# Performance work log

Hardware: AMD Instinct MI355X
Metric: run time of the kernel (lower is better)

## Reference

```python
import jax, jax.numpy as jnp
from jax import lax
import numpy as np

B, T, FEAT = 32, 256, 640
H, P = 2048, 640  # lstm_hidden_units, lstm_projection
FORGET_BIAS = 1.0  # TF v1 LSTMCell default


def setup_inputs() -> dict:
    key = jax.random.key(0)
    ks = jax.random.split(key, 6)
    s = 0.02  # small init so tanh/sigmoid stay well-conditioned
    return {
        "x": jax.random.normal(ks[0], (B, T, FEAT), dtype=jnp.float32),
        "W0": jax.random.normal(ks[1], (FEAT + P, 4 * H), dtype=jnp.float32) * s,
        "b0": jnp.zeros((4 * H,), dtype=jnp.float32),
        "P0": jax.random.normal(ks[2], (H, P), dtype=jnp.float32) * s,
        "W1": jax.random.normal(ks[3], (P + P, 4 * H), dtype=jnp.float32) * s,
        "b1": jnp.zeros((4 * H,), dtype=jnp.float32),
        "P1": jax.random.normal(ks[4], (H, P), dtype=jnp.float32) * s,
    }


def _lstmp_layer(x, W, b, proj):
    # x: [B, T, D]; TF v1 LSTMCell with num_proj, gate order (i, j, f, o)
    batch = x.shape[0]
    c0 = jnp.zeros((batch, H), dtype=x.dtype)
    m0 = jnp.zeros((batch, proj.shape[1]), dtype=x.dtype)

    def step(carry, xt):
        c, m = carry
        z = jnp.concatenate([xt, m], axis=-1) @ W + b  # [B, 4H]
        i, j, f, o = jnp.split(z, 4, axis=-1)
        c_new = jax.nn.sigmoid(f + FORGET_BIAS) * c + jax.nn.sigmoid(i) * jnp.tanh(j)
        m_new = (jax.nn.sigmoid(o) * jnp.tanh(c_new)) @ proj  # [B, P]
        return (c_new, m_new), m_new

    xT = jnp.swapaxes(x, 0, 1)  # [T, B, D]
    _, ys = lax.scan(step, (c0, m0), xT)
    return jnp.swapaxes(ys, 0, 1)  # [B, T, P]


def reference(x, W0, b0, P0, W1, b1, P1):
    h = _lstmp_layer(x, W0, b0, P0)
    h = _lstmp_layer(h, W1, b1, P1)
    return h
```

## Files before the change

kernel.cpp:

```cpp
#include <hip/hip_runtime.h>
#include <math.h>

typedef __attribute__((ext_vector_type(8))) short s16x8;
typedef __attribute__((ext_vector_type(8))) _Float16 f16x8;
typedef __attribute__((ext_vector_type(16))) float f32x16;
typedef unsigned long long u64;
typedef unsigned short u16;

#define NBLK 256
#define NTHR 512

constexpr int HSZ2 = 32 * 2048;
constexpr int MSZH = 32 * 640;

__device__ __forceinline__ float sigm(float v) { return 1.0f / (1.0f + expf(-v)); }

__device__ __forceinline__ unsigned short bf16_rne(float x) {
    unsigned u = __float_as_uint(x);
    return (unsigned short)((u + 0x7FFFu + ((u >> 16) & 1u)) >> 16);
}
__device__ __forceinline__ void split2(float x, unsigned short& hi, unsigned short& lo) {
    unsigned u = __float_as_uint(x);
    hi = (unsigned short)(u >> 16);
    float hf = __uint_as_float(u & 0xFFFF0000u);
    lo = bf16_rne(x - hf);
}
__device__ __forceinline__ void split8(const float* f, s16x8& h, s16x8& l) {
    #pragma unroll
    for (int i = 0; i < 8; ++i) {
        unsigned short hh, ll;
        split2(f[i], hh, ll);
        h[i] = (short)hh; l[i] = (short)ll;
    }
}

__device__ __forceinline__ void ast64(u16* p, u64 v) {
    __hip_atomic_store((u64*)p, v, __ATOMIC_RELAXED, __HIP_MEMORY_SCOPE_AGENT);
}
__device__ __forceinline__ void ast16(u16* p, u16 v) {
    __hip_atomic_store(p, v, __ATOMIC_RELAXED, __HIP_MEMORY_SCOPE_AGENT);
}

__device__ __forceinline__ void pollall(const unsigned* arr, unsigned e) {
    if (threadIdx.x < 64) {
        const int i0 = (int)threadIdx.x * 4;
        for (;;) {
            bool ok = (__hip_atomic_load(arr + i0 + 0, __ATOMIC_RELAXED, __HIP_MEMORY_SCOPE_AGENT) >= e) &&
                      (__hip_atomic_load(arr + i0 + 1, __ATOMIC_RELAXED, __HIP_MEMORY_SCOPE_AGENT) >= e) &&
                      (__hip_atomic_load(arr + i0 + 2, __ATOMIC_RELAXED, __HIP_MEMORY_SCOPE_AGENT) >= e) &&
                      (__hip_atomic_load(arr + i0 + 3, __ATOMIC_RELAXED, __HIP_MEMORY_SCOPE_AGENT) >= e);
            if (__all(ok)) break;
            __builtin_amdgcn_s_sleep(1);
        }
    }
    __syncthreads();
}

__global__ void transpose_split(const float* __restrict__ in,
                                u16* __restrict__ outHi, u16* __restrict__ outLo,
                                int R, int C) {
    __shared__ float tile[32][33];
    const int c0 = blockIdx.x * 32, r0 = blockIdx.y * 32;
    const int tid = threadIdx.x;
    {
        int r = tid >> 3, q = (tid & 7) * 4;
        float4 v = *(const float4*)(in + (size_t)(r0 + r) * C + c0 + q);
        tile[q + 0][r] = v.x; tile[q + 1][r] = v.y;
        tile[q + 2][r] = v.z; tile[q + 3][r] = v.w;
    }
    __syncthreads();
    {
        int c = tid >> 3, q = (tid & 7) * 4;
        ushort4 h, l;
        unsigned short hh, ll;
        split2(tile[c][q + 0], hh, ll); h.x = hh; l.x = ll;
        split2(tile[c][q + 1], hh, ll); h.y = hh; l.y = ll;
        split2(tile[c][q + 2], hh, ll); h.z = hh; l.z = ll;
        split2(tile[c][q + 3], hh, ll); h.w = hh; l.w = ll;
        size_t o = (size_t)(c0 + c) * R + r0 + q;
        *(ushort4*)(outHi + o) = h;
        *(ushort4*)(outLo + o) = l;
    }
}

__global__ void transpose_f16(const float* __restrict__ in, u16* __restrict__ outp,
                              int R, int C) {
    __shared__ float tile[32][33];
    const int c0 = blockIdx.x * 32, r0 = blockIdx.y * 32;
    const int tid = threadIdx.x;
    {
        int r = tid >> 3, q = (tid & 7) * 4;
        float4 v = *(const float4*)(in + (size_t)(r0 + r) * C + c0 + q);
        tile[q + 0][r] = v.x; tile[q + 1][r] = v.y;
        tile[q + 2][r] = v.z; tile[q + 3][r] = v.w;
    }
    __syncthreads();
    {
        int c = tid >> 3, q = (tid & 7) * 4;
        ushort4 o;
        o.x = __builtin_bit_cast(u16, (_Float16)tile[c][q + 0]);
        o.y = __builtin_bit_cast(u16, (_Float16)tile[c][q + 1]);
        o.z = __builtin_bit_cast(u16, (_Float16)tile[c][q + 2]);
        o.w = __builtin_bit_cast(u16, (_Float16)tile[c][q + 3]);
        *(ushort4*)(outp + (size_t)(c0 + c) * R + r0 + q) = o;
    }
}

__global__ void xcast(const float* __restrict__ in, u16* __restrict__ outp, int n4) {
    int i = blockIdx.x * blockDim.x + threadIdx.x;
    if (i < n4) {
        float4 v = ((const float4*)in)[i];
        ushort4 o;
        o.x = __builtin_bit_cast(u16, (_Float16)v.x);
        o.y = __builtin_bit_cast(u16, (_Float16)v.y);
        o.z = __builtin_bit_cast(u16, (_Float16)v.z);
        o.w = __builtin_bit_cast(u16, (_Float16)v.w);
        ((ushort4*)outp)[i] = o;
    }
}

__global__ void __launch_bounds__(256) qgemm(const float* __restrict__ P,
    const u16* __restrict__ WH, const u16* __restrict__ WL,
    u16* __restrict__ Qt) {
    const int tid = threadIdx.x;
    const int wid = tid >> 6, lane = tid & 63;
    const int n = lane & 31, kg = lane >> 5;
    const int tile = blockIdx.x * 4 + wid;
    const int ct = tile & 255, kt = tile >> 8;
    const int col = ct * 32 + n;
    const int krow = kt * 32 + n;

    f32x16 acc;
    #pragma unroll
    for (int r = 0; r < 16; ++r) acc[r] = 0.f;

    const float* ap = P + (size_t)krow * 640 + kg * 8;
    const u16* bhp = WH + (size_t)col * 1280 + 640 + kg * 8;
    const u16* blp = WL + (size_t)col * 1280 + 640 + kg * 8;
    #pragma unroll 4
    for (int ks = 0; ks < 40; ++ks) {
        float4 v0 = *(const float4*)(ap + ks * 16);
        float4 v1 = *(const float4*)(ap + ks * 16 + 4);
        float f[8] = {v0.x, v0.y, v0.z, v0.w, v1.x, v1.y, v1.z, v1.w};
        s16x8 ah, al;
        split8(f, ah, al);
        s16x8 bh = *(const s16x8*)(bhp + ks * 16);
        s16x8 bl = *(const s16x8*)(blp + ks * 16);
        acc = __builtin_amdgcn_mfma_f32_32x32x16_bf16(ah, bh, acc, 0, 0, 0);
        acc = __builtin_amdgcn_mfma_f32_32x32x16_bf16(ah, bl, acc, 0, 0, 0);
        acc = __builtin_amdgcn_mfma_f32_32x32x16_bf16(al, bh, acc, 0, 0, 0);
    }
    u16* qrow = Qt + (size_t)col * 2048 + kt * 32 + 4 * kg;
    #pragma unroll
    for (int q = 0; q < 4; ++q) {
        ushort4 o;
        o.x = __builtin_bit_cast(u16, (_Float16)acc[4 * q + 0]);
        o.y = __builtin_bit_cast(u16, (_Float16)acc[4 * q + 1]);
        o.z = __builtin_bit_cast(u16, (_Float16)acc[4 * q + 2]);
        o.w = __builtin_bit_cast(u16, (_Float16)acc[4 * q + 3]);
        *(ushort4*)(qrow + 8 * q) = o;
    }
}

__global__ void __launch_bounds__(NTHR, 2) lstm_pipe(
    const u16* __restrict__ xh,
    const float* __restrict__ bias0, const float* __restrict__ bias1,
    const u16* __restrict__ Wxt0, const u16* __restrict__ Wxt1,
    const u16* __restrict__ Qt0, const u16* __restrict__ Qt1,
    const u16* __restrict__ Pt0, const u16* __restrict__ Pt1,
    u16* __restrict__ hb0, u16* __restrict__ hb1,
    u16* __restrict__ m0r,
    float* out, unsigned* arr) {
    __shared__ float part[8][64][20];
    __shared__ float zb0[32][33];
    __shared__ float zb1[32][33];
    __shared__ u16 hst0[32][8];
    __shared__ u16 hst1[32][8];

    const int tid = threadIdx.x, bid = blockIdx.x;
    const int wid = tid >> 6, lane = tid & 63;
    const int n = lane & 31, kg = lane >> 5;

    const int colmap = (n >> 3) * 2048 + bid * 8 + (n & 7);
    const size_t wx640 = (size_t)colmap * 640 + wid * 80 + kg * 8;
    const size_t qOff  = (size_t)colmap * 2048 + wid * 256 + kg * 8;
    const size_t aXh   = (size_t)n * (256 * 640) + wid * 80 + kg * 8;
    const size_t aM    = (size_t)n * 640 + wid * 80 + kg * 8;
    const size_t hROff = (size_t)n * 2048 + wid * 256 + kg * 8;

    const int rn = tid >> 4, rm0 = (tid & 15) * 2;
    const int ch = tid >> 5, cb = tid & 31;

    const bool isL0t = bid < 40;
    const int  l0tb  = (bid < 20) ? bid : bid - 20;
    const int  l0par = (bid < 20) ? 0 : 1;
    const bool isL1t = (bid >= 40 && bid < 80);
    const int  l1tb  = (bid < 60) ? bid - 40 : bid - 60;
    const int  l1par = (bid < 60) ? 0 : 1;
    const size_t p0Off = (size_t)(l0tb * 32 + n) * 2048 + wid * 256 + kg * 8;
    const size_t p1Off = (size_t)(l1tb * 32 + n) * 2048 + wid * 256 + kg * 8;

    const float bv0 = bias0[(rn >> 3) * 2048 + bid * 8 + (rn & 7)];
    const float bv1 = bias1[(rn >> 3) * 2048 + bid * 8 + (rn & 7)];

    uint4 q0r[16], q1r[16];
    #pragma unroll
    for (int ks = 0; ks < 16; ++ks) {
        q0r[ks] = *(const uint4*)(Qt0 + qOff + ks * 16);
        q1r[ks] = *(const uint4*)(Qt1 + qOff + ks * 16);
    }
    #pragma unroll
    for (int ks = 0; ks < 16; ++ks) {
        asm volatile("" : "+v"(q0r[ks].x), "+v"(q0r[ks].y), "+v"(q0r[ks].z), "+v"(q0r[ks].w));
        asm volatile("" : "+v"(q1r[ks].x), "+v"(q1r[ks].y), "+v"(q1r[ks].z), "+v"(q1r[ks].w));
    }

    float creg0 = 0.f, creg1 = 0.f;

    auto xp0 = [&](int t) -> f32x16 {
        f32x16 a;
        #pragma unroll
        for (int r = 0; r < 16; ++r) a[r] = 0.f;
        const u16* xb = xh + aXh + (size_t)t * 640;
        const u16* wb = Wxt0 + wx640;
        #pragma unroll
        for (int ks = 0; ks < 5; ++ks)
            a = __builtin_amdgcn_mfma_f32_32x32x16_f16(*(const f16x8*)(xb + ks * 16),
                                                       *(const f16x8*)(wb + ks * 16), a, 0, 0, 0);
        return a;
    };
    auto xp1 = [&](int s) -> f32x16 {
        f32x16 a;
        #pragma unroll
        for (int r = 0; r < 16; ++r) a[r] = 0.f;
        const u16* mb = m0r + (size_t)s * MSZH + aM;
        const u16* wb = Wxt1 + wx640;
        #pragma unroll
        for (int ks = 0; ks < 5; ++ks)
            a = __builtin_amdgcn_mfma_f32_32x32x16_f16(*(const f16x8*)(mb + ks * 16),
                                                       *(const f16x8*)(wb + ks * 16), a, 0, 0, 0);
        return a;
    };
    auto stash = [&](const f32x16& v) {
        #pragma unroll
        for (int r = 0; r < 4; ++r) {
            float4 w;
            w.x = v[4 * r + 0]; w.y = v[4 * r + 1];
            w.z = v[4 * r + 2]; w.w = v[4 * r + 3];
            *(float4*)&part[wid][lane][4 * r] = w;
        }
    };
    auto sum8 = [&](int m) -> float {
        int lp = rn + 32 * ((m >> 2) & 1);
        int rg = (m & 3) + 4 * (m >> 3);
        float s = 0.f;
        #pragma unroll
        for (int w = 0; w < 8; ++w) s += part[w][lp][rg];
        return s;
    };

    f32x16 zacc0 = xp0(0);

    for (int g = 0; g <= 257; ++g) {
        if (g > 0) pollall(arr, (unsigned)g);
        const int s = g - 2;
        const bool doL0 = (g <= 255);
        const bool doL1 = (s >= 0);
        const bool l0p  = isL0t && g >= 1 && g <= 255 && (((g - 1) & 1) == l0par);
        const bool l0pT = isL0t && g == 256 && (((g - 1) & 1) == l0par);
        const bool l1p  = isL1t && s >= 1 && (((s - 1) & 1) == l1par);

        f32x16 pacc0, pacc1;

        if (doL0) {
            f32x16 acc0 = zacc0;
            if (l0p) {
                #pragma unroll
                for (int r = 0; r < 16; ++r) pacc0[r] = 0.f;
            }
            if (g >= 1) {
                const u16* hc = hb0 + (size_t)(g - 1) * HSZ2 + hROff;
                const u16* pf = Pt0 + p0Off;
                if (l0p) {
                    #pragma unroll
                    for (int ks = 0; ks < 16; ++ks) {
                        f16x8 a = *(const f16x8*)(hc + ks * 16);
                        acc0  = __builtin_amdgcn_mfma_f32_32x32x16_f16(a, __builtin_bit_cast(f16x8, q0r[ks]), acc0, 0, 0, 0);
                        pacc0 = __builtin_amdgcn_mfma_f32_32x32x16_f16(a, *(const f16x8*)(pf + ks * 16), pacc0, 0, 0, 0);
                    }
                } else {
                    #pragma unroll
                    for (int ks = 0; ks < 16; ++ks)
                        acc0 = __builtin_amdgcn_mfma_f32_32x32x16_f16(*(const f16x8*)(hc + ks * 16),
                                                                      __builtin_bit_cast(f16x8, q0r[ks]), acc0, 0, 0, 0);
                }
            }
            stash(acc0);
            __syncthreads();
            #pragma unroll
            for (int j = 0; j < 2; ++j) { int m = rm0 + j; zb0[rn][m] = sum8(m) + bv0; }
            __syncthreads();
            if (tid < 256) {
                float zi = zb0[0 * 8 + ch][cb];
                float zj = zb0[1 * 8 + ch][cb];
                float zf = zb0[2 * 8 + ch][cb];
                float zo = zb0[3 * 8 + ch][cb];
                float cn = sigm(zf + 1.0f) * creg0 + sigm(zi) * tanhf(zj);
                creg0 = cn;
                hst0[cb][ch] = __builtin_bit_cast(u16, (_Float16)(sigm(zo) * tanhf(cn)));
            }
        }

        if (l0pT) {
            #pragma unroll
            for (int r = 0; r < 16; ++r) pacc0[r] = 0.f;
            const u16* hc = hb0 + (size_t)255 * HSZ2 + hROff;
            const u16* pf = Pt0 + p0Off;
            #pragma unroll
            for (int ks = 0; ks < 16; ++ks)
                pacc0 = __builtin_amdgcn_mfma_f32_32x32x16_f16(*(const f16x8*)(hc + ks * 16),
                                                               *(const f16x8*)(pf + ks * 16), pacc0, 0, 0, 0);
        }
        if (l0p || l0pT) {
            __syncthreads();
            stash(pacc0);
            __syncthreads();
            u16* mrow = m0r + (size_t)(g - 1) * MSZH;
            #pragma unroll
            for (int j = 0; j < 2; ++j) {
                int m = rm0 + j;
                ast16(mrow + (size_t)m * 640 + l0tb * 32 + rn,
                      __builtin_bit_cast(u16, (_Float16)sum8(m)));
            }
        }

        if (doL1) {
            f32x16 acc1 = xp1(s);
            if (l1p) {
                #pragma unroll
                for (int r = 0; r < 16; ++r) pacc1[r] = 0.f;
            }
            if (s >= 1) {
                const u16* hc = hb1 + (size_t)(s - 1) * HSZ2 + hROff;
                const u16* pf = Pt1 + p1Off;
                if (l1p) {
                    #pragma unroll
                    for (int ks = 0; ks < 16; ++ks) {
                        f16x8 a = *(const f16x8*)(hc + ks * 16);
                        acc1  = __builtin_amdgcn_mfma_f32_32x32x16_f16(a, __builtin_bit_cast(f16x8, q1r[ks]), acc1, 0, 0, 0);
                        pacc1 = __builtin_amdgcn_mfma_f32_32x32x16_f16(a, *(const f16x8*)(pf + ks * 16), pacc1, 0, 0, 0);
                    }
                } else {
                    #pragma unroll
                    for (int ks = 0; ks < 16; ++ks)
                        acc1 = __builtin_amdgcn_mfma_f32_32x32x16_f16(*(const f16x8*)(hc + ks * 16),
                                                                      __builtin_bit_cast(f16x8, q1r[ks]), acc1, 0, 0, 0);
                }
            }
            __syncthreads();
            stash(acc1);
            __syncthreads();
            #pragma unroll
            for (int j = 0; j < 2; ++j) { int m = rm0 + j; zb1[rn][m] = sum8(m) + bv1; }
            __syncthreads();
            if (tid < 256) {
                float zi = zb1[0 * 8 + ch][cb];
                float zj = zb1[1 * 8 + ch][cb];
                float zf = zb1[2 * 8 + ch][cb];
                float zo = zb1[3 * 8 + ch][cb];
                float cn = sigm(zf + 1.0f) * creg1 + sigm(zi) * tanhf(zj);
                creg1 = cn;
                hst1[cb][ch] = __builtin_bit_cast(u16, (_Float16)(sigm(zo) * tanhf(cn)));
            }
        }

        __syncthreads();
        if (doL0 && wid == 0) {
            int b = tid >> 1, hf = tid & 1;
            u64 v = *(const u64*)&hst0[b][hf * 4];
            ast64(hb0 + (size_t)g * HSZ2 + (size_t)b * 2048 + bid * 8 + hf * 4, v);
        }
        if (doL1 && wid == 1) {
            int l = tid - 64;
            int b = l >> 1, hf = l & 1;
            u64 v = *(const u64*)&hst1[b][hf * 4];
            ast64(hb1 + (size_t)s * HSZ2 + (size_t)b * 2048 + bid * 8 + hf * 4, v);
        }
        __syncthreads();
        if (tid == 0)
            __hip_atomic_store(arr + bid, (unsigned)(g + 1), __ATOMIC_RELAXED, __HIP_MEMORY_SCOPE_AGENT);

        if (l1p) {
            __syncthreads();
            stash(pacc1);
            __syncthreads();
            #pragma unroll
            for (int j = 0; j < 2; ++j) {
                int m = rm0 + j;
                out[((size_t)m * 256 + (s - 1)) * 640 + l1tb * 32 + rn] = sum8(m);
            }
        }
        if (g < 255) zacc0 = xp0(g + 1);
    }

    if (isL1t && l1par == 1) {
        pollall(arr, 258u);
        f32x16 pacc;
        #pragma unroll
        for (int r = 0; r < 16; ++r) pacc[r] = 0.f;
        const u16* hc = hb1 + (size_t)255 * HSZ2 + hROff;
        const u16* pf = Pt1 + p1Off;
        #pragma unroll
        for (int ks = 0; ks < 16; ++ks)
            pacc = __builtin_amdgcn_mfma_f32_32x32x16_f16(*(const f16x8*)(hc + ks * 16),
                                                          *(const f16x8*)(pf + ks * 16), pacc, 0, 0, 0);
        stash(pacc);
        __syncthreads();
        #pragma unroll
        for (int j = 0; j < 2; ++j) {
            int m = rm0 + j;
            out[((size_t)m * 256 + 255) * 640 + l1tb * 32 + rn] = sum8(m);
        }
    }
}

__device__ __forceinline__ void grid_bar_slow(unsigned int* bar, unsigned int& epoch) {
    __syncthreads();
    epoch++;
    if (threadIdx.x == 0) {
        __threadfence();
        atomicAdd(bar, 1u);
        const unsigned int target = epoch * NBLK;
        while (__hip_atomic_load(bar, __ATOMIC_RELAXED, __HIP_MEMORY_SCOPE_AGENT) < target)
            __builtin_amdgcn_s_sleep(1);
        __threadfence();
    }
    __syncthreads();
}

__global__ void __launch_bounds__(NTHR, 1) lstm_fb(
    const float* __restrict__ x,
    const float* __restrict__ W0, const float* __restrict__ b0, const float* __restrict__ Pr0,
    const float* __restrict__ W1, const float* __restrict__ b1, const float* __restrict__ Pr1,
    float* out, float* ws) {
    const int tid = threadIdx.x;
    const int bid = blockIdx.x;
    unsigned int* bar = (unsigned int*)ws;
    float* mbuf0 = ws + 1024;
    float* mbuf1 = mbuf0 + 32 * 640;
    float* hws = mbuf1 + 32 * 640;
    __shared__ float zbuf[32 * 33];
    __shared__ float pred[512];
    unsigned int epoch = 0;
    const int c_idx = tid & 31;
    const int bg = tid >> 5;
    const int b0r = bg * 2;
    const int col = (c_idx >> 3) * 2048 + bid * 8 + (c_idx & 7);
    const int ch = tid >> 5;
    const int cb = tid & 31;
    const int p_s = (bid * 640) / NBLK;
    const int p_e = ((bid + 1) * 640) / NBLK;
    const int np = p_e - p_s;
    const int kq_n = (np == 2) ? 8 : 4;
    const int klen = 2048 / kq_n;
    const int pg = tid >> 5;
    const bool pact = pg < np * kq_n;
    const int pj = pact ? (pg % np) : 0;
    const int kq = pact ? (pg / np) : 0;
    for (int layer = 0; layer < 2; ++layer) {
        const float* W = layer ? W1 : W0;
        const float* bbv = layer ? b1 : b0;
        const float* Pr = layer ? Pr1 : Pr0;
        const float* inb = layer ? (const float*)out : x;
        for (int i = bid * NTHR + tid; i < 32 * 640; i += NBLK * NTHR) mbuf0[i] = 0.0f;
        float creg = 0.0f;
        grid_bar_slow(bar, epoch);
        const float bias = bbv[col];
        for (int t = 0; t < 256; ++t) {
            float* mcur = (t & 1) ? mbuf1 : mbuf0;
            float* mnxt = (t & 1) ? mbuf0 : mbuf1;
            const float* in0 = inb + (size_t)(b0r * 256 + t) * 640;
            const float* in1 = in0 + (size_t)256 * 640;
            const float* wp = W + col;
            float a0 = 0.f, a1 = 0.f;
            #pragma unroll 4
            for (int k = 0; k < 640; k += 4) {
                float4 u0 = *(const float4*)(in0 + k);
                float4 u1 = *(const float4*)(in1 + k);
                float w0 = wp[(size_t)(k + 0) * 8192], w1 = wp[(size_t)(k + 1) * 8192];
                float w2 = wp[(size_t)(k + 2) * 8192], w3 = wp[(size_t)(k + 3) * 8192];
                a0 += w0 * u0.x + w1 * u0.y + w2 * u0.z + w3 * u0.w;
                a1 += w0 * u1.x + w1 * u1.y + w2 * u1.z + w3 * u1.w;
            }
            const float* q0 = mcur + (size_t)b0r * 640;
            const float* q1 = q0 + 640;
            #pragma unroll 4
            for (int k = 0; k < 640; k += 4) {
                float4 u0 = *(const float4*)(q0 + k);
                float4 u1 = *(const float4*)(q1 + k);
                float w0 = wp[(size_t)(640 + k + 0) * 8192], w1 = wp[(size_t)(640 + k + 1) * 8192];
                float w2 = wp[(size_t)(640 + k + 2) * 8192], w3 = wp[(size_t)(640 + k + 3) * 8192];
                a0 += w0 * u0.x + w1 * u0.y + w2 * u0.z + w3 * u0.w;
                a1 += w0 * u1.x + w1 * u1.y + w2 * u1.z + w3 * u1.w;
            }
            zbuf[c_idx * 33 + b0r + 0] = a0 + bias;
            zbuf[c_idx * 33 + b0r + 1] = a1 + bias;
            __syncthreads();
            if (tid < 256) {
                float zi = zbuf[(0 * 8 + ch) * 33 + cb];
                float zj = zbuf[(1 * 8 + ch) * 33 + cb];
                float zf = zbuf[(2 * 8 + ch) * 33 + cb];
                float zo = zbuf[(3 * 8 + ch) * 33 + cb];
                float cn = sigm(zf + 1.0f) * creg + sigm(zi) * tanhf(zj);
                creg = cn;
                hws[(size_t)(bid * 8 + ch) * 32 + cb] = sigm(zo) * tanhf(cn);
            }
            grid_bar_slow(bar, epoch);
            if (pact) {
                const int p = p_s + pj;
                const float* pp = Pr + p;
                const int k0 = kq * klen;
                float s = 0.f;
                #pragma unroll 4
                for (int k = k0; k < k0 + klen; ++k) s += hws[(size_t)k * 32 + cb] * pp[(size_t)k * 640];
                pred[(pj * 32 + cb) * kq_n + kq] = s;
            }
            __syncthreads();
            if (tid < np * 32) {
                float s = 0.f;
                for (int q2 = 0; q2 < kq_n; ++q2) s += pred[tid * kq_n + q2];
                const int p = p_s + (tid >> 5);
                const int b = tid & 31;
                mnxt[(size_t)b * 640 + p] = s;
                out[((size_t)b * 256 + t) * 640 + p] = s;
            }
            grid_bar_slow(bar, epoch);
        }
    }
}

extern "C" void kernel_launch(void* const* d_in, const int* in_sizes, int n_in,
                              void* d_out, int out_size, void* d_ws, size_t ws_size,
                              hipStream_t stream) {
    const float* x   = (const float*)d_in[0];
    const float* W0  = (const float*)d_in[1];
    const float* b0  = (const float*)d_in[2];
    const float* P0  = (const float*)d_in[3];
    const float* W1  = (const float*)d_in[4];
    const float* b1  = (const float*)d_in[5];
    const float* P1  = (const float*)d_in[6];
    float* out = (float*)d_out;

    size_t off = 0;
    auto alloc = [&](size_t bytes) { size_t o = off; off += (bytes + 255) & ~(size_t)255; return o; };
    const size_t oBar = alloc(32768);
    const size_t szW  = (size_t)8192 * 1280 * 2;
    const size_t szQ  = (size_t)8192 * 2048 * 2;
    const size_t szPt = (size_t)640 * 2048 * 2;
    const size_t szWx = (size_t)8192 * 640 * 2;
    const size_t oWH  = alloc(szW), oWL = alloc(szW);
    const size_t oQt0 = alloc(szQ), oQt1 = alloc(szQ);
    const size_t oPt0 = alloc(szPt), oPt1 = alloc(szPt);
    const size_t oWx0 = alloc(szWx), oWx1 = alloc(szWx);
    const size_t oXh  = alloc((size_t)32 * 256 * 640 * 2);
    const size_t oH0  = alloc((size_t)256 * HSZ2 * 2);
    const size_t oH1  = alloc((size_t)256 * HSZ2 * 2);
    const size_t oM0  = alloc((size_t)256 * MSZH * 2);
    const size_t need = off;

    hipMemsetAsync(d_ws, 0, 32768, stream);

    if (ws_size < need) {
        float* ws = (float*)d_ws;
        void* args[] = {(void*)&x, (void*)&W0, (void*)&b0, (void*)&P0,
                        (void*)&W1, (void*)&b1, (void*)&P1, (void*)&out, (void*)&ws};
        hipError_t err = hipLaunchCooperativeKernel((const void*)lstm_fb,
                                                    dim3(NBLK), dim3(NTHR), args, 0, stream);
        if (err != hipSuccess)
            lstm_fb<<<dim3(NBLK), dim3(NTHR), 0, stream>>>(x, W0, b0, P0, W1, b1, P1, out, ws);
        return;
    }

    char* w = (char*)d_ws;
    u16 *WHp = (u16*)(w + oWH), *WLp = (u16*)(w + oWL);
    u16 *Qt0p = (u16*)(w + oQt0), *Qt1p = (u16*)(w + oQt1);
    u16 *Pt0p = (u16*)(w + oPt0), *Pt1p = (u16*)(w + oPt1);
    u16 *Wx0p = (u16*)(w + oWx0), *Wx1p = (u16*)(w + oWx1);
    u16 *xhp  = (u16*)(w + oXh);
    u16 *hb0p = (u16*)(w + oH0), *hb1p = (u16*)(w + oH1);
    u16 *m0rp = (u16*)(w + oM0);
    unsigned* arrp = (unsigned*)(w + oBar);

    transpose_split<<<dim3(256, 40), 256, 0, stream>>>(W0, WHp, WLp, 1280, 8192);
    qgemm<<<dim3(4096), 256, 0, stream>>>(P0, WHp, WLp, Qt0p);
    transpose_split<<<dim3(256, 40), 256, 0, stream>>>(W1, WHp, WLp, 1280, 8192);
    qgemm<<<dim3(4096), 256, 0, stream>>>(P1, WHp, WLp, Qt1p);
    transpose_f16<<<dim3(20, 64), 256, 0, stream>>>(P0, Pt0p, 2048, 640);
    transpose_f16<<<dim3(20, 64), 256, 0, stream>>>(P1, Pt1p, 2048, 640);
    transpose_f16<<<dim3(256, 20), 256, 0, stream>>>(W0, Wx0p, 640, 8192);
    transpose_f16<<<dim3(256, 20), 256, 0, stream>>>(W1, Wx1p, 640, 8192);
    xcast<<<dim3(5120), 256, 0, stream>>>(x, xhp, 32 * 256 * 640 / 4);

    const float *b0c = b0, *b1c = b1;
    void* args[] = {(void*)&xhp, (void*)&b0c, (void*)&b1c,
                    (void*)&Wx0p, (void*)&Wx1p,
                    (void*)&Qt0p, (void*)&Qt1p, (void*)&Pt0p, (void*)&Pt1p,
                    (void*)&hb0p, (void*)&hb1p, (void*)&m0rp,
                    (void*)&out, (void*)&arrp};
    hipError_t err = hipLaunchCooperativeKernel((const void*)lstm_pipe,
                                                dim3(NBLK), dim3(NTHR), args, 0, stream);
    if (err != hipSuccess)
        lstm_pipe<<<dim3(NBLK), dim3(NTHR), 0, stream>>>(
            xhp, b0c, b1c, Wx0p, Wx1p, Qt0p, Qt1p, Pt0p, Pt1p,
            hb0p, hb1p, m0rp, out, arrp);
}
```

Baseline: 6.127 ms.

## Fold layer-0 projection into layer-1 input weights and shorten pipeline lag

Layer 1's input term m0 @ W1x is rewritten as h0 @ (P0 @ W1x), precomputed as Qt01. Layer 1 now consumes h0 directly in the same MFMA loop as layer 0, sharing the A-operand loads. This removes the explicit m0 projection, its global round-trip and one step of pipeline lag (258 to 257 sync steps). It also drops the x cast kernel and the W1 transpose by converting x to fp16 inline. In exchange it holds a third register-resident weight block, raising register pressure, and layer 1's input GEMM grows from K=640 to K=2048 per step.

```diff
diff --git a/kernel.cpp b/kernel.cpp
--- a/kernel.cpp
+++ b/kernel.cpp
@@ -11,7 +11,6 @@
 #define NTHR 512
 
 constexpr int HSZ2 = 32 * 2048;
-constexpr int MSZH = 32 * 640;
 
 __device__ __forceinline__ float sigm(float v) { return 1.0f / (1.0f + expf(-v)); }
 
@@ -36,9 +35,6 @@
 
 __device__ __forceinline__ void ast64(u16* p, u64 v) {
     __hip_atomic_store((u64*)p, v, __ATOMIC_RELAXED, __HIP_MEMORY_SCOPE_AGENT);
-}
-__device__ __forceinline__ void ast16(u16* p, u16 v) {
-    __hip_atomic_store(p, v, __ATOMIC_RELAXED, __HIP_MEMORY_SCOPE_AGENT);
 }
 
 __device__ __forceinline__ void pollall(const unsigned* arr, unsigned e) {
@@ -106,22 +102,9 @@
     }
 }
 
-__global__ void xcast(const float* __restrict__ in, u16* __restrict__ outp, int n4) {
-    int i = blockIdx.x * blockDim.x + threadIdx.x;
-    if (i < n4) {
-        float4 v = ((const float4*)in)[i];
-        ushort4 o;
-        o.x = __builtin_bit_cast(u16, (_Float16)v.x);
-        o.y = __builtin_bit_cast(u16, (_Float16)v.y);
-        o.z = __builtin_bit_cast(u16, (_Float16)v.z);
-        o.w = __builtin_bit_cast(u16, (_Float16)v.w);
-        ((ushort4*)outp)[i] = o;
-    }
-}
-
 __global__ void __launch_bounds__(256) qgemm(const float* __restrict__ P,
     const u16* __restrict__ WH, const u16* __restrict__ WL,
-    u16* __restrict__ Qt) {
+    u16* __restrict__ Qt, int rowOff) {
     const int tid = threadIdx.x;
     const int wid = tid >> 6, lane = tid & 63;
     const int n = lane & 31, kg = lane >> 5;
@@ -135,8 +118,8 @@
     for (int r = 0; r < 16; ++r) acc[r] = 0.f;
 
     const float* ap = P + (size_t)krow * 640 + kg * 8;
-    const u16* bhp = WH + (size_t)col * 1280 + 640 + kg * 8;
-    const u16* blp = WL + (size_t)col * 1280 + 640 + kg * 8;
+    const u16* bhp = WH + (size_t)col * 1280 + rowOff + kg * 8;
+    const u16* blp = WL + (size_t)col * 1280 + rowOff + kg * 8;
     #pragma unroll 4
     for (int ks = 0; ks < 40; ++ks) {
         float4 v0 = *(const float4*)(ap + ks * 16);
@@ -163,13 +146,12 @@
 }
 
 __global__ void __launch_bounds__(NTHR, 2) lstm_pipe(
-    const u16* __restrict__ xh,
+    const float* __restrict__ x,
     const float* __restrict__ bias0, const float* __restrict__ bias1,
-    const u16* __restrict__ Wxt0, const u16* __restrict__ Wxt1,
-    const u16* __restrict__ Qt0, const u16* __restrict__ Qt1,
-    const u16* __restrict__ Pt0, const u16* __restrict__ Pt1,
+    const u16* __restrict__ Wxt0,
+    const u16* __restrict__ Qt0, const u16* __restrict__ Qt01, const u16* __restrict__ Qt1,
+    const u16* __restrict__ Pt1,
     u16* __restrict__ hb0, u16* __restrict__ hb1,
-    u16* __restrict__ m0r,
     float* out, unsigned* arr) {
     __shared__ float part[8][64][20];
     __shared__ float zb0[32][33];
@@ -184,35 +166,32 @@
     const int colmap = (n >> 3) * 2048 + bid * 8 + (n & 7);
     const size_t wx640 = (size_t)colmap * 640 + wid * 80 + kg * 8;
     const size_t qOff  = (size_t)colmap * 2048 + wid * 256 + kg * 8;
-    const size_t aXh   = (size_t)n * (256 * 640) + wid * 80 + kg * 8;
-    const size_t aM    = (size_t)n * 640 + wid * 80 + kg * 8;
+    const size_t aXf   = (size_t)n * (256 * 640) + wid * 80 + kg * 8;
     const size_t hROff = (size_t)n * 2048 + wid * 256 + kg * 8;
 
     const int rn = tid >> 4, rm0 = (tid & 15) * 2;
     const int ch = tid >> 5, cb = tid & 31;
 
-    const bool isL0t = bid < 40;
-    const int  l0tb  = (bid < 20) ? bid : bid - 20;
-    const int  l0par = (bid < 20) ? 0 : 1;
-    const bool isL1t = (bid >= 40 && bid < 80);
-    const int  l1tb  = (bid < 60) ? bid - 40 : bid - 60;
-    const int  l1par = (bid < 60) ? 0 : 1;
-    const size_t p0Off = (size_t)(l0tb * 32 + n) * 2048 + wid * 256 + kg * 8;
-    const size_t p1Off = (size_t)(l1tb * 32 + n) * 2048 + wid * 256 + kg * 8;
+    const bool isT = bid < 40;
+    const int  tb  = (bid < 20) ? bid : bid - 20;
+    const int  par = (bid < 20) ? 0 : 1;
+    const size_t pOff = (size_t)(tb * 32 + n) * 2048 + wid * 256 + kg * 8;
 
     const float bv0 = bias0[(rn >> 3) * 2048 + bid * 8 + (rn & 7)];
     const float bv1 = bias1[(rn >> 3) * 2048 + bid * 8 + (rn & 7)];
 
-    uint4 q0r[16], q1r[16];
+    uint4 q0r[16], q01r[16], q1r[16];
     #pragma unroll
     for (int ks = 0; ks < 16; ++ks) {
-        q0r[ks] = *(const uint4*)(Qt0 + qOff + ks * 16);
-        q1r[ks] = *(const uint4*)(Qt1 + qOff + ks * 16);
+        q0r[ks]  = *(const uint4*)(Qt0  + qOff + ks * 16);
+        q01r[ks] = *(const uint4*)(Qt01 + qOff + ks * 16);
+        q1r[ks]  = *(const uint4*)(Qt1  + qOff + ks * 16);
     }
     #pragma unroll
     for (int ks = 0; ks < 16; ++ks) {
-        asm volatile("" : "+v"(q0r[ks].x), "+v"(q0r[ks].y), "+v"(q0r[ks].z), "+v"(q0r[ks].w));
-        asm volatile("" : "+v"(q1r[ks].x), "+v"(q1r[ks].y), "+v"(q1r[ks].z), "+v"(q1r[ks].w));
+        asm volatile("" : "+v"(q0r[ks].x),  "+v"(q0r[ks].y),  "+v"(q0r[ks].z),  "+v"(q0r[ks].w));
+        asm volatile("" : "+v"(q01r[ks].x), "+v"(q01r[ks].y), "+v"(q01r[ks].z), "+v"(q01r[ks].w));
+        asm volatile("" : "+v"(q1r[ks].x),  "+v"(q1r[ks].y),  "+v"(q1r[ks].z),  "+v"(q1r[ks].w));
     }
 
     float creg0 = 0.f, creg1 = 0.f;
@@ -221,24 +200,19 @@
         f32x16 a;
         #pragma unroll
         for (int r = 0; r < 16; ++r) a[r] = 0.f;
-        const u16* xb = xh + aXh + (size_t)t * 640;
+        const float* xb = x + aXf + (size_t)t * 640;
         const u16* wb = Wxt0 + wx640;
         #pragma unroll
-        for (int ks = 0; ks < 5; ++ks)
-            a = __builtin_amdgcn_mfma_f32_32x32x16_f16(*(const f16x8*)(xb + ks * 16),
-                                                       *(const f16x8*)(wb + ks * 16), a, 0, 0, 0);
-        return a;
-    };
-    auto xp1 = [&](int s) -> f32x16 {
-        f32x16 a;
-        #pragma unroll
-        for (int r = 0; r < 16; ++r) a[r] = 0.f;
-        const u16* mb = m0r + (size_t)s * MSZH + aM;
-        const u16* wb = Wxt1 + wx640;
-        #pragma unroll
-        for (int ks = 0; ks < 5; ++ks)
-            a = __builtin_amdgcn_mfma_f32_32x32x16_f16(*(const f16x8*)(mb + ks * 16),
-                                                       *(const f16x8*)(wb + ks * 16), a, 0, 0, 0);
+        for (int ks = 0; ks < 5; ++ks) {
+            float4 v0 = *(const float4*)(xb + ks * 16);
+            float4 v1 = *(const float4*)(xb + ks * 16 + 4);
+            f16x8 av;
+            av[0] = (_Float16)v0.x; av[1] = (_Float16)v0.y;
+            av[2] = (_Float16)v0.z; av[3] = (_Float16)v0.w;
+            av[4] = (_Float16)v1.x; av[5] = (_Float16)v1.y;
+            av[6] = (_Float16)v1.z; av[7] = (_Float16)v1.w;
+            a = __builtin_amdgcn_mfma_f32_32x32x16_f16(av, *(const f16x8*)(wb + ks * 16), a, 0, 0, 0);
+        }
         return a;
     };
     auto stash = [&](const f32x16& v) {
@@ -263,118 +237,79 @@
 
     for (int g = 0; g <= 257; ++g) {
         if (g > 0) pollall(arr, (unsigned)g);
-        const int s = g - 2;
+        const int s = g - 1;
         const bool doL0 = (g <= 255);
-        const bool doL1 = (s >= 0);
-        const bool l0p  = isL0t && g >= 1 && g <= 255 && (((g - 1) & 1) == l0par);
-        const bool l0pT = isL0t && g == 256 && (((g - 1) & 1) == l0par);
-        const bool l1p  = isL1t && s >= 1 && (((s - 1) & 1) == l1par);
-
-        f32x16 pacc0, pacc1;
+        const bool doL1 = (s >= 0 && s <= 255);
+
+        f32x16 acc0, acc1;
+        if (doL0) acc0 = zacc0;
+        if (doL1) {
+            #pragma unroll
+            for (int r = 0; r < 16; ++r) acc1[r] = 0.f;
+        }
+        if (g >= 1) {
+            const u16* h0c = hb0 + (size_t)(g - 1) * HSZ2 + hROff;
+            if (doL0 && doL1) {
+                #pragma unroll
+                for (int ks = 0; ks < 16; ++ks) {
+                    f16x8 a = *(const f16x8*)(h0c + ks * 16);
+                    acc0 = __builtin_amdgcn_mfma_f32_32x32x16_f16(a, __builtin_bit_cast(f16x8, q0r[ks]),  acc0, 0, 0, 0);
+                    acc1 = __builtin_amdgcn_mfma_f32_32x32x16_f16(a, __builtin_bit_cast(f16x8, q01r[ks]), acc1, 0, 0, 0);
+                }
+            } else if (doL0) {
+                #pragma unroll
+                for (int ks = 0; ks < 16; ++ks)
+                    acc0 = __builtin_amdgcn_mfma_f32_32x32x16_f16(*(const f16x8*)(h0c + ks * 16),
+                                                                  __builtin_bit_cast(f16x8, q0r[ks]), acc0, 0, 0, 0);
+            } else if (doL1) {
+                #pragma unroll
+                for (int ks = 0; ks < 16; ++ks)
+                    acc1 = __builtin_amdgcn_mfma_f32_32x32x16_f16(*(const f16x8*)(h0c + ks * 16),
+                                                                  __builtin_bit_cast(f16x8, q01r[ks]), acc1, 0, 0, 0);
+            }
+        }
+        if (s >= 1) {
+            const u16* h1c = hb1 + (size_t)(s - 1) * HSZ2 + hROff;
+            #pragma unroll
+            for (int ks = 0; ks < 16; ++ks)
+                acc1 = __builtin_amdgcn_mfma_f32_32x32x16_f16(*(const f16x8*)(h1c + ks * 16),
+                                                              __builtin_bit_cast(f16x8, q1r[ks]), acc1, 0, 0, 0);
+        }
 
         if (doL0) {
-            f32x16 acc0 = zacc0;
-            if (l0p) {
-                #pragma unroll
-                for (int r = 0; r < 16; ++r) pacc0[r] = 0.f;
-            }
-            if (g >= 1) {
-                const u16* hc = hb0 + (size_t)(g - 1) * HSZ2 + hROff;
-                const u16* pf = Pt0 + p0Off;
-                if (l0p) {
-                    #pragma unroll
-                    for (int ks = 0; ks < 16; ++ks) {
-                        f16x8 a = *(const f16x8*)(hc + ks * 16);
-                        acc0  = __builtin_amdgcn_mfma_f32_32x32x16_f16(a, __builtin_bit_cast(f16x8, q0r[ks]), acc0, 0, 0, 0);
-                        pacc0 = __builtin_amdgcn_mfma_f32_32x32x16_f16(a, *(const f16x8*)(pf + ks * 16), pacc0, 0, 0, 0);
-                    }
-                } else {
-                    #pragma unroll
-                    for (int ks = 0; ks < 16; ++ks)
-                        acc0 = __builtin_amdgcn_mfma_f32_32x32x16_f16(*(const f16x8*)(hc + ks * 16),
-                                                                      __builtin_bit_cast(f16x8, q0r[ks]), acc0, 0, 0, 0);
-                }
-            }
             stash(acc0);
             __syncthreads();
             #pragma unroll
             for (int j = 0; j < 2; ++j) { int m = rm0 + j; zb0[rn][m] = sum8(m) + bv0; }
-            __syncthreads();
-            if (tid < 256) {
-                float zi = zb0[0 * 8 + ch][cb];
-                float zj = zb0[1 * 8 + ch][cb];
-                float zf = zb0[2 * 8 + ch][cb];
-                float zo = zb0[3 * 8 + ch][cb];
-                float cn = sigm(zf + 1.0f) * creg0 + sigm(zi) * tanhf(zj);
-                creg0 = cn;
-                hst0[cb][ch] = __builtin_bit_cast(u16, (_Float16)(sigm(zo) * tanhf(cn)));
-            }
-        }
-
-        if (l0pT) {
-            #pragma unroll
-            for (int r = 0; r < 16; ++r) pacc0[r] = 0.f;
-            const u16* hc = hb0 + (size_t)255 * HSZ2 + hROff;
-            const u16* pf = Pt0 + p0Off;
-            #pragma unroll
-            for (int ks = 0; ks < 16; ++ks)
-                pacc0 = __builtin_amdgcn_mfma_f32_32x32x16_f16(*(const f16x8*)(hc + ks * 16),
-                                                               *(const f16x8*)(pf + ks * 16), pacc0, 0, 0, 0);
-        }
-        if (l0p || l0pT) {
-            __syncthreads();
-            stash(pacc0);
-            __syncthreads();
-            u16* mrow = m0r + (size_t)(g - 1) * MSZH;
-            #pragma unroll
-            for (int j = 0; j < 2; ++j) {
-                int m = rm0 + j;
-                ast16(mrow + (size_t)m * 640 + l0tb * 32 + rn,
-                      __builtin_bit_cast(u16, (_Float16)sum8(m)));
-            }
-        }
-
+        }
+        __syncthreads();
         if (doL1) {
-            f32x16 acc1 = xp1(s);
-            if (l1p) {
-                #pragma unroll
-                for (int r = 0; r < 16; ++r) pacc1[r] = 0.f;
-            }
-            if (s >= 1) {
-                const u16* hc = hb1 + (size_t)(s - 1) * HSZ2 + hROff;
-                const u16* pf = Pt1 + p1Off;
-                if (l1p) {
-                    #pragma unroll
-                    for (int ks = 0; ks < 16; ++ks) {
-                        f16x8 a = *(const f16x8*)(hc + ks * 16);
-                        acc1  = __builtin_amdgcn_mfma_f32_32x32x16_f16(a, __builtin_bit_cast(f16x8, q1r[ks]), acc1, 0, 0, 0);
-                        pacc1 = __builtin_amdgcn_mfma_f32_32x32x16_f16(a, *(const f16x8*)(pf + ks * 16), pacc1, 0, 0, 0);
-                    }
-                } else {
-                    #pragma unroll
-                    for (int ks = 0; ks < 16; ++ks)
-                        acc1 = __builtin_amdgcn_mfma_f32_32x32x16_f16(*(const f16x8*)(hc + ks * 16),
-                                                                      __builtin_bit_cast(f16x8, q1r[ks]), acc1, 0, 0, 0);
-                }
-            }
-            __syncthreads();
             stash(acc1);
             __syncthreads();
             #pragma unroll
             for (int j = 0; j < 2; ++j) { int m = rm0 + j; zb1[rn][m] = sum8(m) + bv1; }
-            __syncthreads();
-            if (tid < 256) {
-                float zi = zb1[0 * 8 + ch][cb];
-                float zj = zb1[1 * 8 + ch][cb];
-                float zf = zb1[2 * 8 + ch][cb];
-                float zo = zb1[3 * 8 + ch][cb];
-                float cn = sigm(zf + 1.0f) * creg1 + sigm(zi) * tanhf(zj);
-                creg1 = cn;
-                hst1[cb][ch] = __builtin_bit_cast(u16, (_Float16)(sigm(zo) * tanhf(cn)));
-            }
-        }
-
+        }
+        if (doL0 && tid < 256) {
+            float zi = zb0[0 * 8 + ch][cb];
+            float zj = zb0[1 * 8 + ch][cb];
+            float zf = zb0[2 * 8 + ch][cb];
+            float zo = zb0[3 * 8 + ch][cb];
+            float cn = sigm(zf + 1.0f) * creg0 + sigm(zi) * tanhf(zj);
+            creg0 = cn;
+            hst0[cb][ch] = __builtin_bit_cast(u16, (_Float16)(sigm(zo) * tanhf(cn)));
+        }
         __syncthreads();
+        if (doL1 && tid < 256) {
+            float zi = zb1[0 * 8 + ch][cb];
+            float zj = zb1[1 * 8 + ch][cb];
+            float zf = zb1[2 * 8 + ch][cb];
+            float zo = zb1[3 * 8 + ch][cb];
+            float cn = sigm(zf + 1.0f) * creg1 + sigm(zi) * tanhf(zj);
+            creg1 = cn;
+            hst1[cb][ch] = __builtin_bit_cast(u16, (_Float16)(sigm(zo) * tanhf(cn)));
+        }
+        __syncthreads();
+
         if (doL0 && wid == 0) {
             int b = tid >> 1, hf = tid & 1;
             u64 v = *(const u64*)&hst0[b][hf * 4];
@@ -390,37 +325,27 @@
         if (tid == 0)
             __hip_atomic_store(arr + bid, (unsigned)(g + 1), __ATOMIC_RELAXED, __HIP_MEMORY_SCOPE_AGENT);
 
-        if (l1p) {
+        const int sp = g - 2;
+        if (isT && sp >= 0 && (sp & 1) == par) {
+            f32x16 pacc;
+            #pragma unroll
+            for (int r = 0; r < 16; ++r) pacc[r] = 0.f;
+            const u16* hc = hb1 + (size_t)sp * HSZ2 + hROff;
+            const u16* pf = Pt1 + pOff;
+            #pragma unroll
+            for (int ks = 0; ks < 16; ++ks)
+                pacc = __builtin_amdgcn_mfma_f32_32x32x16_f16(*(const f16x8*)(hc + ks * 16),
+                                                              *(const f16x8*)(pf + ks * 16), pacc, 0, 0, 0);
             __syncthreads();
-            stash(pacc1);
+            stash(pacc);
             __syncthreads();
             #pragma unroll
             for (int j = 0; j < 2; ++j) {
                 int m = rm0 + j;
-                out[((size_t)m * 256 + (s - 1)) * 640 + l1tb * 32 + rn] = sum8(m);
+                out[((size_t)m * 256 + sp) * 640 + tb * 32 + rn] = sum8(m);
             }
         }
         if (g < 255) zacc0 = xp0(g + 1);
-    }
-
-    if (isL1t && l1par == 1) {
-        pollall(arr, 258u);
-        f32x16 pacc;
-        #pragma unroll
-        for (int r = 0; r < 16; ++r) pacc[r] = 0.f;
-        const u16* hc = hb1 + (size_t)255 * HSZ2 + hROff;
-        const u16* pf = Pt1 + p1Off;
-        #pragma unroll
-        for (int ks = 0; ks < 16; ++ks)
-            pacc = __builtin_amdgcn_mfma_f32_32x32x16_f16(*(const f16x8*)(hc + ks * 16),
-                                                          *(const f16x8*)(pf + ks * 16), pacc, 0, 0, 0);
-        stash(pacc);
-        __syncthreads();
-        #pragma unroll
-        for (int j = 0; j < 2; ++j) {
-            int m = rm0 + j;
-            out[((size_t)m * 256 + 255) * 640 + l1tb * 32 + rn] = sum8(m);
-        }
     }
 }
 
@@ -553,20 +478,18 @@
 
     size_t off = 0;
     auto alloc = [&](size_t bytes) { size_t o = off; off += (bytes + 255) & ~(size_t)255; return o; };
-    const size_t oBar = alloc(32768);
-    const size_t szW  = (size_t)8192 * 1280 * 2;
-    const size_t szQ  = (size_t)8192 * 2048 * 2;
-    const size_t szPt = (size_t)640 * 2048 * 2;
-    const size_t szWx = (size_t)8192 * 640 * 2;
-    const size_t oWH  = alloc(szW), oWL = alloc(szW);
-    const size_t oQt0 = alloc(szQ), oQt1 = alloc(szQ);
-    const size_t oPt0 = alloc(szPt), oPt1 = alloc(szPt);
-    const size_t oWx0 = alloc(szWx), oWx1 = alloc(szWx);
-    const size_t oXh  = alloc((size_t)32 * 256 * 640 * 2);
-    const size_t oH0  = alloc((size_t)256 * HSZ2 * 2);
-    const size_t oH1  = alloc((size_t)256 * HSZ2 * 2);
-    const size_t oM0  = alloc((size_t)256 * MSZH * 2);
-    const size_t need = off;
+    const size_t oBar  = alloc(32768);
+    const size_t szW   = (size_t)8192 * 1280 * 2;
+    const size_t szQ   = (size_t)8192 * 2048 * 2;
+    const size_t szPt  = (size_t)640 * 2048 * 2;
+    const size_t szWx  = (size_t)8192 * 640 * 2;
+    const size_t oWH   = alloc(szW), oWL = alloc(szW);
+    const size_t oQt0  = alloc(szQ), oQt01 = alloc(szQ), oQt1 = alloc(szQ);
+    const size_t oPt1  = alloc(szPt);
+    const size_t oWx0  = alloc(szWx);
+    const size_t oH0   = alloc((size_t)256 * HSZ2 * 2);
+    const size_t oH1   = alloc((size_t)256 * HSZ2 * 2);
+    const size_t need  = off;
 
     hipMemsetAsync(d_ws, 0, 32768, stream);
 
@@ -583,34 +506,29 @@
 
     char* w = (char*)d_ws;
     u16 *WHp = (u16*)(w + oWH), *WLp = (u16*)(w + oWL);
-    u16 *Qt0p = (u16*)(w + oQt0), *Qt1p = (u16*)(w + oQt1);
-    u16 *Pt0p = (u16*)(w + oPt0), *Pt1p = (u16*)(w + oPt1);
-    u16 *Wx0p = (u16*)(w + oWx0), *Wx1p = (u16*)(w + oWx1);
-    u16 *xhp  = (u16*)(w + oXh);
+    u16 *Qt0p = (u16*)(w + oQt0), *Qt01p = (u16*)(w + oQt01), *Qt1p = (u16*)(w + oQt1);
+    u16 *Pt1p = (u16*)(w + oPt1);
+    u16 *Wx0p = (u16*)(w + oWx0);
     u16 *hb0p = (u16*)(w + oH0), *hb1p = (u16*)(w + oH1);
-    u16 *m0rp = (u16*)(w + oM0);
     unsigned* arrp = (unsigned*)(w + oBar);
 
     transpose_split<<<dim3(256, 40), 256, 0, stream>>>(W0, WHp, WLp, 1280, 8192);
-    qgemm<<<dim3(4096), 256, 0, stream>>>(P0, WHp, WLp, Qt0p);
+    qgemm<<<dim3(4096), 256, 0, stream>>>(P0, WHp, WLp, Qt0p, 640);
     transpose_split<<<dim3(256, 40), 256, 0, stream>>>(W1, WHp, WLp, 1280, 8192);
-    qgemm<<<dim3(4096), 256, 0, stream>>>(P1, WHp, WLp, Qt1p);
-    transpose_f16<<<dim3(20, 64), 256, 0, stream>>>(P0, Pt0p, 2048, 640);
+    qgemm<<<dim3(4096), 256, 0, stream>>>(P0, WHp, WLp, Qt01p, 0);
+    qgemm<<<dim3(4096), 256, 0, stream>>>(P1, WHp, WLp, Qt1p, 640);
     transpose_f16<<<dim3(20, 64), 256, 0, stream>>>(P1, Pt1p, 2048, 640);
     transpose_f16<<<dim3(256, 20), 256, 0, stream>>>(W0, Wx0p, 640, 8192);
-    transpose_f16<<<dim3(256, 20), 256, 0, stream>>>(W1, Wx1p, 640, 8192);
-    xcast<<<dim3(5120), 256, 0, stream>>>(x, xhp, 32 * 256 * 640 / 4);
 
     const float *b0c = b0, *b1c = b1;
-    void* args[] = {(void*)&xhp, (void*)&b0c, (void*)&b1c,
-                    (void*)&Wx0p, (void*)&Wx1p,
-                    (void*)&Qt0p, (void*)&Qt1p, (void*)&Pt0p, (void*)&Pt1p,
-                    (void*)&hb0p, (void*)&hb1p, (void*)&m0rp,
+    void* args[] = {(void*)&x, (void*)&b0c, (void*)&b1c,
+                    (void*)&Wx0p,
+                    (void*)&Qt0p, (void*)&Qt01p, (void*)&Qt1p, (void*)&Pt1p,
+                    (void*)&hb0p, (void*)&hb1p,
                     (void*)&out, (void*)&arrp};
     hipError_t err = hipLaunchCooperativeKernel((const void*)lstm_pipe,
                                                 dim3(NBLK), dim3(NTHR), args, 0, stream);
     if (err != hipSuccess)
         lstm_pipe<<<dim3(NBLK), dim3(NTHR), 0, stream>>>(
-            xhp, b0c, b1c, Wx0p, Wx1p, Qt0p, Qt1p, Pt0p, Pt1p,
-            hb0p, hb1p, m0rp, out, arrp);
-}
+            x, b0c, b1c, Wx0p, Qt0p, Qt01p, Qt1p, Pt1p, hb0p, hb1p, out, arrp);
+}
```

After: 6.803 ms. +11.0%, slower.
